# Kernel tuning notes

Hardware: AMD Instinct MI355X
Metric: run time of the kernel (lower is better)

The kernel has to match this reference:

```python
import jax, jax.numpy as jnp
import numpy as np

N = 50000
E = 800000
IN_DIM = 128
HID = 128
OUT = 40


def setup_inputs() -> dict:
    key = jax.random.key(0)
    k1, k2, k3, k4, k5 = jax.random.split(key, 5)
    x = jax.random.normal(k1, (N, IN_DIM), dtype=jnp.float32)
    edge_index = jax.random.randint(k2, (2, E), 0, N, dtype=jnp.int64)
    # Glorot-ish init for GCNConv weights, zero bias (PyG default bias=True)
    W1 = jax.random.normal(k3, (IN_DIM, HID), dtype=jnp.float32) / np.sqrt(IN_DIM)
    b1 = jnp.zeros((HID,), dtype=jnp.float32)
    W2 = jax.random.normal(k4, (HID, OUT), dtype=jnp.float32) / np.sqrt(HID)
    b2 = jnp.zeros((OUT,), dtype=jnp.float32)
    return {"x": x, "edge_index": edge_index, "W1": W1, "b1": b1, "W2": W2, "b2": b2}


def _gcn_norm(edge_index, n_nodes):
    """Add self-loops and compute symmetric GCN normalization per edge.
    Returns (src, dst, norm) with len E + n_nodes."""
    loops = jnp.arange(n_nodes, dtype=edge_index.dtype)
    src = jnp.concatenate([edge_index[0], loops])
    dst = jnpp_concat = jnp.concatenate([edge_index[1], loops])
    dst = jnp.concatenate([edge_index[1], loops])
    deg = jax.ops.segment_sum(jnp.ones_like(dst, dtype=jnp.float32), dst,
                              num_segments=n_nodes)
    dinv = jnp.where(deg > 0, jax.lax.rsqrt(deg), 0.0)
    norm = dinv[src] * dinv[dst]  # [E + N]
    return src, dst, norm


def _gcn_conv(x, src, dst, norm, W, b, n_nodes):
    xw = x @ W                                  # [N, F_out] transform first
    msg = xw[src] * norm[:, None]               # gather + scale, [E+N, F_out]
    out = jax.ops.segment_sum(msg, dst, num_segments=n_nodes)  # scatter-add
    return out + b


def reference(x, edge_index, W1, b1, W2, b2):
    n = x.shape[0]
    src, dst, norm = _gcn_norm(edge_index, n)
    h = _gcn_conv(x, src, dst, norm, W1, b1, n)
    h = jax.nn.relu(h)
    # dropout is identity in eval mode (training=False)
    h = _gcn_conv(h, src, dst, norm, W2, b2, n)
    return jax.nn.softmax(h, axis=1)
```

## Files before the change

kernel.cpp:

```cpp
#include <hip/hip_runtime.h>
#include <hip/hip_fp16.h>

#define IN_DIM 128
#define HID    128
#define OUTC   40
#define CAP    64
#define LSTR   136
#define CHUNK  4096
#define BINCAP 800

typedef _Float16 f16x8 __attribute__((ext_vector_type(8)));
typedef _Float16 f16x4 __attribute__((ext_vector_type(4)));
typedef float    f32x4 __attribute__((ext_vector_type(4)));

__device__ __forceinline__ int permi(int d, int NP8) { return (d & 7) * NP8 + (d >> 3); }

__global__ __launch_bounds__(256) void k_part(const int* __restrict__ edge, unsigned* __restrict__ staging,
                                              int* __restrict__ gcnt,
                                              const float* __restrict__ W1, const float* __restrict__ W2,
                                              _Float16* __restrict__ W1T, _Float16* __restrict__ W2T,
                                              int E, int n, int nbA, int ES8) {
  int b = blockIdx.x;
  if (b >= nbA) {
    int t = (b - nbA) * 256 + threadIdx.x;
    if (t < 128 * 128) {
      int nn = t >> 7, kk = t & 127;
      W1T[t] = (_Float16)W1[kk * 128 + nn];
    }
    if (t < 48 * 128) {
      int nn = t >> 7, kk = t & 127;
      W2T[t] = (nn < OUTC) ? (_Float16)W2[kk * OUTC + nn] : (_Float16)0.f;
    }
    return;
  }
  __shared__ unsigned lbin[8][BINCAP];
  __shared__ int lcnt[8];
  __shared__ int lbase[8];
  int tid = threadIdx.x;
  if (tid < 8) lcnt[tid] = 0;
  __syncthreads();
  int e0 = b * CHUNK;
#pragma unroll 4
  for (int i = 0; i < CHUNK / 256; ++i) {
    int e = e0 + i * 256 + tid;
    if (e < E) {
      int sv = edge[e];
      int d  = edge[E + e];
      if ((unsigned)d < (unsigned)n && (unsigned)sv < (unsigned)n) {
        int g = d & 7;
        unsigned pk = ((unsigned)(d >> 3) << 16) | (unsigned)sv;
        int p = atomicAdd(&lcnt[g], 1);
        if (p < BINCAP) lbin[g][p] = pk;
        else {
          int gp = atomicAdd(&gcnt[g], 1);
          staging[(size_t)g * ES8 + gp] = pk;
        }
      }
    }
  }
  __syncthreads();
  if (tid < 8) lbase[tid] = atomicAdd(&gcnt[tid], min(lcnt[tid], BINCAP));
  __syncthreads();
#pragma unroll
  for (int g = 0; g < 8; ++g) {
    int c = min(lcnt[g], BINCAP);
    int base = lbase[g];
    for (int idx = tid; idx < c; idx += 256)
      staging[(size_t)g * ES8 + base + idx] = lbin[g][idx];
  }
}

__global__ __launch_bounds__(256) void k_scat(const unsigned* __restrict__ staging, const int* __restrict__ gcnt,
                                              int* __restrict__ cnt, unsigned short* __restrict__ col,
                                              int NP8, int ES8) {
  int g = blockIdx.x & 7;
  int cE = gcnt[g];
  int t       = (blockIdx.x >> 3) * 256 + threadIdx.x;
  int gstride = (gridDim.x >> 3) * 256;
  const unsigned* sg = &staging[(size_t)g * ES8];
  for (int i = t; i < cE; i += gstride) {
    unsigned pk = sg[i];
    int p = g * NP8 + (int)(pk >> 16);
    int pos = atomicAdd(&cnt[p], 1);
    if (pos < CAP) col[(size_t)p * CAP + pos] = (unsigned short)(pk & 0xFFFFu);
  }
}


__global__ __launch_bounds__(256) void k_gemm1(const float* __restrict__ x, const _Float16* __restrict__ W1T,
                                               const int* __restrict__ cnt, __half* __restrict__ out,
                                               int n, int NP8) {
  __shared__ _Float16 sW[128 * LSTR];
  __shared__ _Float16 sX[64 * LSTR];
  int tid = threadIdx.x;
  int i0  = blockIdx.x * 64;

  {
    const uint4* src = (const uint4*)W1T;
    for (int idx = tid; idx < 2048; idx += 256) {
      int nn = idx >> 4, c = idx & 15;
      *(uint4*)&sW[nn * LSTR + c * 8] = src[nn * 16 + c];
    }
  }
  for (int idx = tid; idx < 2048; idx += 256) {
    int r = idx >> 5, c = idx & 31;
    int row = i0 + r;
    float4 v = (row < n) ? *(const float4*)&x[(size_t)row * IN_DIM + c * 4]
                         : make_float4(0.f, 0.f, 0.f, 0.f);
    f16x4 hv; hv[0] = (_Float16)v.x; hv[1] = (_Float16)v.y; hv[2] = (_Float16)v.z; hv[3] = (_Float16)v.w;
    *(f16x4*)&sX[r * LSTR + c * 4] = hv;
  }
  __syncthreads();

  int wv = tid >> 6, lane = tid & 63;
  int m = lane & 15, quad = lane >> 4;

  const _Float16* ax = &sX[(16 * wv + m) * LSTR + quad * 8];
  f16x8 a0 = *(const f16x8*)(ax);
  f16x8 a1 = *(const f16x8*)(ax + 32);
  f16x8 a2 = *(const f16x8*)(ax + 64);
  f16x8 a3 = *(const f16x8*)(ax + 96);

  int base_row = i0 + 16 * wv + quad * 4;
  float dvr[4];
#pragma unroll
  for (int r = 0; r < 4; ++r) {
    int row = base_row + r;
    dvr[r] = (row < n) ? rsqrtf((float)(cnt[permi(row, NP8)] + 1)) : 0.f;
  }

#pragma unroll
  for (int t = 0; t < 8; ++t) {
    const _Float16* bx = &sW[(t * 16 + m) * LSTR + quad * 8];
    f16x8 b0 = *(const f16x8*)(bx);
    f16x8 b1 = *(const f16x8*)(bx + 32);
    f16x8 b2 = *(const f16x8*)(bx + 64);
    f16x8 b3 = *(const f16x8*)(bx + 96);
    f32x4 c = {0.f, 0.f, 0.f, 0.f};
    c = __builtin_amdgcn_mfma_f32_16x16x32_f16(a0, b0, c, 0, 0, 0);
    c = __builtin_amdgcn_mfma_f32_16x16x32_f16(a1, b1, c, 0, 0, 0);
    c = __builtin_amdgcn_mfma_f32_16x16x32_f16(a2, b2, c, 0, 0, 0);
    c = __builtin_amdgcn_mfma_f32_16x16x32_f16(a3, b3, c, 0, 0, 0);
    int colb = t * 16 + m;
#pragma unroll
    for (int r = 0; r < 4; ++r) {
      int row = base_row + r;
      if (row < n) out[(size_t)row * HID + colb] = __float2half(c[r] * dvr[r]);
    }
  }
}


__global__ __launch_bounds__(256) void k_agg1(const __half2* __restrict__ xws, const int* __restrict__ cnt,
                                              const unsigned short* __restrict__ col, const float* __restrict__ b1,
                                              __half2* __restrict__ h, int n, int NP8) {
  int wid  = (blockIdx.x * 256 + threadIdx.x) >> 6;
  int lane = threadIdx.x & 63;
  if (wid >= n) return;
  float2 acc = __half22float2(xws[(size_t)wid * 64 + lane]);
  int p   = permi(wid, NP8);
  int deg = cnt[p];
  int end = min(deg, CAP);
  const unsigned short* cp = &col[(size_t)p * CAP];
  int e = 0;
  for (; e + 8 <= end; e += 8) {
    int s0 = cp[e], s1 = cp[e+1], s2 = cp[e+2], s3 = cp[e+3];
    int s4 = cp[e+4], s5 = cp[e+5], s6 = cp[e+6], s7 = cp[e+7];
    float2 v0 = __half22float2(xws[(size_t)s0 * 64 + lane]);
    float2 v1 = __half22float2(xws[(size_t)s1 * 64 + lane]);
    float2 v2 = __half22float2(xws[(size_t)s2 * 64 + lane]);
    float2 v3 = __half22float2(xws[(size_t)s3 * 64 + lane]);
    float2 v4 = __half22float2(xws[(size_t)s4 * 64 + lane]);
    float2 v5 = __half22float2(xws[(size_t)s5 * 64 + lane]);
    float2 v6 = __half22float2(xws[(size_t)s6 * 64 + lane]);
    float2 v7 = __half22float2(xws[(size_t)s7 * 64 + lane]);
    acc.x += (v0.x + v1.x) + (v2.x + v3.x) + ((v4.x + v5.x) + (v6.x + v7.x));
    acc.y += (v0.y + v1.y) + (v2.y + v3.y) + ((v4.y + v5.y) + (v6.y + v7.y));
  }
  for (; e < end; ++e) {
    float2 v = __half22float2(xws[(size_t)cp[e] * 64 + lane]);
    acc.x += v.x; acc.y += v.y;
  }
  float dv = rsqrtf((float)(deg + 1));
  float2 bb = ((const float2*)b1)[lane];
  h[(size_t)wid * 64 + lane] =
      __floats2half2_rn(fmaxf(acc.x * dv + bb.x, 0.f), fmaxf(acc.y * dv + bb.y, 0.f));
}


__global__ __launch_bounds__(256) void k_gemm2(const __half* __restrict__ h, const _Float16* __restrict__ W2T,
                                               const int* __restrict__ cnt, __half* __restrict__ out,
                                               int n, int NP8) {
  __shared__ _Float16 sW[48 * LSTR];
  __shared__ _Float16 sH[64 * LSTR];
  int tid = threadIdx.x;
  int i0  = blockIdx.x * 64;

  {
    const uint4* src = (const uint4*)W2T;
    for (int idx = tid; idx < 768; idx += 256) {
      int nn = idx >> 4, c = idx & 15;
      *(uint4*)&sW[nn * LSTR + c * 8] = src[nn * 16 + c];
    }
  }
  {
    const uint4* src = (const uint4*)h;
    for (int idx = tid; idx < 1024; idx += 256) {
      int r = idx >> 4, c = idx & 15;
      int row = i0 + r;
      uint4 v = (row < n) ? src[(size_t)row * 16 + c] : make_uint4(0u, 0u, 0u, 0u);
      *(uint4*)&sH[r * LSTR + c * 8] = v;
    }
  }
  __syncthreads();

  int wv = tid >> 6, lane = tid & 63;
  int m = lane & 15, quad = lane >> 4;

  const _Float16* ax = &sH[(16 * wv + m) * LSTR + quad * 8];
  f16x8 a0 = *(const f16x8*)(ax);
  f16x8 a1 = *(const f16x8*)(ax + 32);
  f16x8 a2 = *(const f16x8*)(ax + 64);
  f16x8 a3 = *(const f16x8*)(ax + 96);

  int base_row = i0 + 16 * wv + quad * 4;
  float dvr[4];
#pragma unroll
  for (int r = 0; r < 4; ++r) {
    int row = base_row + r;
    dvr[r] = (row < n) ? rsqrtf((float)(cnt[permi(row, NP8)] + 1)) : 0.f;
  }

#pragma unroll
  for (int t = 0; t < 3; ++t) {
    const _Float16* bx = &sW[(t * 16 + m) * LSTR + quad * 8];
    f16x8 b0 = *(const f16x8*)(bx);
    f16x8 b1 = *(const f16x8*)(bx + 32);
    f16x8 b2 = *(const f16x8*)(bx + 64);
    f16x8 b3 = *(const f16x8*)(bx + 96);
    f32x4 c = {0.f, 0.f, 0.f, 0.f};
    c = __builtin_amdgcn_mfma_f32_16x16x32_f16(a0, b0, c, 0, 0, 0);
    c = __builtin_amdgcn_mfma_f32_16x16x32_f16(a1, b1, c, 0, 0, 0);
    c = __builtin_amdgcn_mfma_f32_16x16x32_f16(a2, b2, c, 0, 0, 0);
    c = __builtin_amdgcn_mfma_f32_16x16x32_f16(a3, b3, c, 0, 0, 0);
    int colb = t * 16 + m;
    if (colb < OUTC) {
#pragma unroll
      for (int r = 0; r < 4; ++r) {
        int row = base_row + r;
        if (row < n) out[(size_t)row * OUTC + colb] = __float2half(c[r] * dvr[r]);
      }
    }
  }
}


__global__ __launch_bounds__(256) void k_agg2(const __half* __restrict__ hw, const int* __restrict__ cnt,
                                              const unsigned short* __restrict__ col, const float* __restrict__ b2,
                                              float* __restrict__ out, int n, int NP8) {
  int wid  = (blockIdx.x * 256 + threadIdx.x) >> 6;
  int lane = threadIdx.x & 63;
  if (wid >= n) return;
  bool act = lane < OUTC;
  int li = act ? lane : 0;
  float acc = act ? __half2float(hw[(size_t)wid * OUTC + li]) : 0.f;
  int p   = permi(wid, NP8);
  int deg = cnt[p];
  int end = min(deg, CAP);
  const unsigned short* cp = &col[(size_t)p * CAP];
  int e = 0;
  for (; e + 8 <= end; e += 8) {
    int s0 = cp[e], s1 = cp[e+1], s2 = cp[e+2], s3 = cp[e+3];
    int s4 = cp[e+4], s5 = cp[e+5], s6 = cp[e+6], s7 = cp[e+7];
    if (act) {
      float a0 = __half2float(hw[(size_t)s0 * OUTC + li]);
      float a1 = __half2float(hw[(size_t)s1 * OUTC + li]);
      float a2 = __half2float(hw[(size_t)s2 * OUTC + li]);
      float a3 = __half2float(hw[(size_t)s3 * OUTC + li]);
      float a4 = __half2float(hw[(size_t)s4 * OUTC + li]);
      float a5 = __half2float(hw[(size_t)s5 * OUTC + li]);
      float a6 = __half2float(hw[(size_t)s6 * OUTC + li]);
      float a7 = __half2float(hw[(size_t)s7 * OUTC + li]);
      acc += (a0 + a1) + (a2 + a3) + ((a4 + a5) + (a6 + a7));
    }
  }
  for (; e < end; ++e) {
    int s = cp[e];
    if (act) acc += __half2float(hw[(size_t)s * OUTC + li]);
  }
  float logit = acc * rsqrtf((float)(deg + 1)) + (act ? b2[lane] : 0.f);
  float m = act ? logit : -1e30f;
#pragma unroll
  for (int o = 32; o > 0; o >>= 1) m = fmaxf(m, __shfl_xor(m, o, 64));
  float ex = act ? __expf(logit - m) : 0.f;
  float sum = ex;
#pragma unroll
  for (int o = 32; o > 0; o >>= 1) sum += __shfl_xor(sum, o, 64);
  if (act) out[(size_t)wid * OUTC + lane] = ex / sum;
}


extern "C" void kernel_launch(void* const* d_in, const int* in_sizes, int n_in,
                              void* d_out, int out_size, void* d_ws, size_t ws_size,
                              hipStream_t stream) {
  const float* x    = (const float*)d_in[0];
  const int*   edge = (const int*)d_in[1];
  const float* W1   = (const float*)d_in[2];
  const float* b1   = (const float*)d_in[3];
  const float* W2   = (const float*)d_in[4];
  const float* b2   = (const float*)d_in[5];
  float* out = (float*)d_out;

  int N   = in_sizes[0] / IN_DIM;
  int E   = in_sizes[1] / 2;
  int NP8 = (N + 7) / 8;
  int NP  = NP8 * 8;
  int ES8 = E / 8 + 16384;

  char* ws = (char*)d_ws;
  size_t off = 0;
  auto carve = [&](size_t bytes) { char* p = ws + off; off = (off + bytes + 255) & ~(size_t)255; return p; };
  int*            gcnt    = (int*)carve(8 * 4);
  int*            cnt     = (int*)carve((size_t)NP * 4);
  unsigned*       staging = (unsigned*)carve((size_t)8 * ES8 * 4);
  unsigned short* col     = (unsigned short*)carve((size_t)NP * CAP * 2);
  _Float16*       W1T     = (_Float16*)carve((size_t)128 * 128 * 2);
  _Float16*       W2T     = (_Float16*)carve((size_t)48 * 128 * 2);
  __half*         xws     = (__half*)carve((size_t)N * HID * 2);
  __half*         h       = (__half*)carve((size_t)N * HID * 2);
  __half*         hw      = xws;

  hipMemsetAsync(gcnt, 0, (size_t)((char*)staging - (char*)gcnt), stream);

  int nbA = (E + CHUNK - 1) / CHUNK;
  k_part<<<nbA + 64, 256, 0, stream>>>(edge, staging, gcnt, W1, W2, W1T, W2T, E, N, nbA, ES8);
  k_scat<<<512, 256, 0, stream>>>(staging, gcnt, cnt, col, NP8, ES8);

  k_gemm1<<<(N + 63) / 64, 256, 0, stream>>>(x, W1T, cnt, xws, N, NP8);
  k_agg1<<<(N * 64 + 255) / 256, 256, 0, stream>>>((const __half2*)xws, cnt, col, b1, (__half2*)h, N, NP8);
  k_gemm2<<<(N + 63) / 64, 256, 0, stream>>>(h, W2T, cnt, hw, N, NP8);
  k_agg2<<<(N * 64 + 255) / 256, 256, 0, stream>>>(hw, cnt, col, b2, out, N, NP8);
}
```

Before: 222.5 us.

## Fuse edge partitioning with GEMM1 and aggregation1 with GEMM2

GEMM1 now runs in the same launch as edge partitioning, so it no longer scales by source degree. The missing scaling is applied per neighbor during aggregation by reading each source's degree. Layer-1 aggregation is fused with the layer-2 GEMM so the hidden activations stay in shared memory instead of round-tripping through global memory. A small init kernel replaces the memset, and the partition and GEMM1 work overlap in a single launch. In exchange, aggregation does an extra random cnt read and rsqrt per edge, and each block handles 64 rows with only 4 waves, which reduces parallelism for the gather.

```diff
diff --git a/kernel.cpp b/kernel.cpp
--- a/kernel.cpp
+++ b/kernel.cpp
@@ -15,58 +15,122 @@
 
 __device__ __forceinline__ int permi(int d, int NP8) { return (d & 7) * NP8 + (d >> 3); }
 
-__global__ __launch_bounds__(256) void k_part(const int* __restrict__ edge, unsigned* __restrict__ staging,
-                                              int* __restrict__ gcnt,
+__global__ __launch_bounds__(256) void k_init(int* __restrict__ cnt, int NP, int* __restrict__ gcnt,
                                               const float* __restrict__ W1, const float* __restrict__ W2,
-                                              _Float16* __restrict__ W1T, _Float16* __restrict__ W2T,
-                                              int E, int n, int nbA, int ES8) {
-  int b = blockIdx.x;
-  if (b >= nbA) {
-    int t = (b - nbA) * 256 + threadIdx.x;
-    if (t < 128 * 128) {
-      int nn = t >> 7, kk = t & 127;
-      W1T[t] = (_Float16)W1[kk * 128 + nn];
-    }
-    if (t < 48 * 128) {
-      int nn = t >> 7, kk = t & 127;
-      W2T[t] = (nn < OUTC) ? (_Float16)W2[kk * OUTC + nn] : (_Float16)0.f;
-    }
-    return;
-  }
-  __shared__ unsigned lbin[8][BINCAP];
-  __shared__ int lcnt[8];
-  __shared__ int lbase[8];
+                                              _Float16* __restrict__ W1T, _Float16* __restrict__ W2T) {
+  int t = blockIdx.x * 256 + threadIdx.x;
+  int stride = gridDim.x * 256;
+  for (int i = t; i < NP; i += stride) cnt[i] = 0;
+  if (t < 8) gcnt[t] = 0;
+  for (int i = t; i < 128 * 128; i += stride) {
+    int nn = i >> 7, kk = i & 127;
+    W1T[i] = (_Float16)W1[kk * 128 + nn];
+  }
+  for (int i = t; i < 48 * 128; i += stride) {
+    int nn = i >> 7, kk = i & 127;
+    W2T[i] = (nn < OUTC) ? (_Float16)W2[kk * OUTC + nn] : (_Float16)0.f;
+  }
+}
+
+#define SMEM_SZ 52224
+
+__global__ __launch_bounds__(256) void k_part_gemm1(const int* __restrict__ edge, unsigned* __restrict__ staging,
+                                                    int* __restrict__ gcnt,
+                                                    const float* __restrict__ x, const _Float16* __restrict__ W1T,
+                                                    __half* __restrict__ xws,
+                                                    int E, int n, int nbA, int ES8) {
+  __shared__ __align__(16) char smem[SMEM_SZ];
+  int b   = blockIdx.x;
   int tid = threadIdx.x;
-  if (tid < 8) lcnt[tid] = 0;
-  __syncthreads();
-  int e0 = b * CHUNK;
+
+  if (b < nbA) {
+    unsigned (*lbin)[BINCAP] = (unsigned (*)[BINCAP])smem;
+    int* lcnt  = (int*)(smem + 8 * BINCAP * 4);
+    int* lbase = lcnt + 8;
+    if (tid < 8) lcnt[tid] = 0;
+    __syncthreads();
+    int e0 = b * CHUNK;
 #pragma unroll 4
-  for (int i = 0; i < CHUNK / 256; ++i) {
-    int e = e0 + i * 256 + tid;
-    if (e < E) {
-      int sv = edge[e];
-      int d  = edge[E + e];
-      if ((unsigned)d < (unsigned)n && (unsigned)sv < (unsigned)n) {
-        int g = d & 7;
-        unsigned pk = ((unsigned)(d >> 3) << 16) | (unsigned)sv;
-        int p = atomicAdd(&lcnt[g], 1);
-        if (p < BINCAP) lbin[g][p] = pk;
-        else {
-          int gp = atomicAdd(&gcnt[g], 1);
-          staging[(size_t)g * ES8 + gp] = pk;
+    for (int i = 0; i < CHUNK / 256; ++i) {
+      int e = e0 + i * 256 + tid;
+      if (e < E) {
+        int sv = edge[e];
+        int d  = edge[E + e];
+        if ((unsigned)d < (unsigned)n && (unsigned)sv < (unsigned)n) {
+          int g = d & 7;
+          unsigned pk = ((unsigned)(d >> 3) << 16) | (unsigned)sv;
+          int p = atomicAdd(&lcnt[g], 1);
+          if (p < BINCAP) lbin[g][p] = pk;
+          else {
+            int gp = atomicAdd(&gcnt[g], 1);
+            staging[(size_t)g * ES8 + gp] = pk;
+          }
         }
       }
     }
+    __syncthreads();
+    if (tid < 8) lbase[tid] = atomicAdd(&gcnt[tid], min(lcnt[tid], BINCAP));
+    __syncthreads();
+#pragma unroll
+    for (int g = 0; g < 8; ++g) {
+      int c = min(lcnt[g], BINCAP);
+      int base = lbase[g];
+      for (int idx = tid; idx < c; idx += 256)
+        staging[(size_t)g * ES8 + base + idx] = lbin[g][idx];
+    }
+    return;
+  }
+
+  _Float16* sW = (_Float16*)smem;
+  _Float16* sX = (_Float16*)(smem + 128 * LSTR * 2);
+  int i0 = (b - nbA) * 64;
+
+  {
+    const uint4* src = (const uint4*)W1T;
+    for (int idx = tid; idx < 2048; idx += 256) {
+      int nn = idx >> 4, c = idx & 15;
+      *(uint4*)&sW[nn * LSTR + c * 8] = src[nn * 16 + c];
+    }
+  }
+  for (int idx = tid; idx < 2048; idx += 256) {
+    int r = idx >> 5, c = idx & 31;
+    int row = i0 + r;
+    float4 v = (row < n) ? *(const float4*)&x[(size_t)row * IN_DIM + c * 4]
+                         : make_float4(0.f, 0.f, 0.f, 0.f);
+    f16x4 hv; hv[0] = (_Float16)v.x; hv[1] = (_Float16)v.y; hv[2] = (_Float16)v.z; hv[3] = (_Float16)v.w;
+    *(f16x4*)&sX[r * LSTR + c * 4] = hv;
   }
   __syncthreads();
-  if (tid < 8) lbase[tid] = atomicAdd(&gcnt[tid], min(lcnt[tid], BINCAP));
-  __syncthreads();
-#pragma unroll
-  for (int g = 0; g < 8; ++g) {
-    int c = min(lcnt[g], BINCAP);
-    int base = lbase[g];
-    for (int idx = tid; idx < c; idx += 256)
-      staging[(size_t)g * ES8 + base + idx] = lbin[g][idx];
+
+  int wv = tid >> 6, lane = tid & 63;
+  int m = lane & 15, quad = lane >> 4;
+
+  const _Float16* ax = &sX[(16 * wv + m) * LSTR + quad * 8];
+  f16x8 a0 = *(const f16x8*)(ax);
+  f16x8 a1 = *(const f16x8*)(ax + 32);
+  f16x8 a2 = *(const f16x8*)(ax + 64);
+  f16x8 a3 = *(const f16x8*)(ax + 96);
+
+  int base_row = i0 + 16 * wv + quad * 4;
+
+#pragma unroll
+  for (int t = 0; t < 8; ++t) {
+    const _Float16* bx = &sW[(t * 16 + m) * LSTR + quad * 8];
+    f16x8 b0 = *(const f16x8*)(bx);
+    f16x8 b1 = *(const f16x8*)(bx + 32);
+    f16x8 b2 = *(const f16x8*)(bx + 64);
+    f16x8 b3 = *(const f16x8*)(bx + 96);
+    f32x4 c = {0.f, 0.f, 0.f, 0.f};
+    c = __builtin_amdgcn_mfma_f32_16x16x32_f16(a0, b0, c, 0, 0, 0);
+    c = __builtin_amdgcn_mfma_f32_16x16x32_f16(a1, b1, c, 0, 0, 0);
+    c = __builtin_amdgcn_mfma_f32_16x16x32_f16(a2, b2, c, 0, 0, 0);
+    c = __builtin_amdgcn_mfma_f32_16x16x32_f16(a3, b3, c, 0, 0, 0);
+    int colb = t * 16 + m;
+#pragma unroll
+    for (int r = 0; r < 4; ++r) {
+      int row = base_row + r;
+      if (row < n) xws[(size_t)row * HID + colb] = __float2half(c[r]);
+    }
   }
 }
 
@@ -87,112 +151,13 @@
 }
 
 
-__global__ __launch_bounds__(256) void k_gemm1(const float* __restrict__ x, const _Float16* __restrict__ W1T,
-                                               const int* __restrict__ cnt, __half* __restrict__ out,
-                                               int n, int NP8) {
-  __shared__ _Float16 sW[128 * LSTR];
-  __shared__ _Float16 sX[64 * LSTR];
-  int tid = threadIdx.x;
-  int i0  = blockIdx.x * 64;
-
-  {
-    const uint4* src = (const uint4*)W1T;
-    for (int idx = tid; idx < 2048; idx += 256) {
-      int nn = idx >> 4, c = idx & 15;
-      *(uint4*)&sW[nn * LSTR + c * 8] = src[nn * 16 + c];
-    }
-  }
-  for (int idx = tid; idx < 2048; idx += 256) {
-    int r = idx >> 5, c = idx & 31;
-    int row = i0 + r;
-    float4 v = (row < n) ? *(const float4*)&x[(size_t)row * IN_DIM + c * 4]
-                         : make_float4(0.f, 0.f, 0.f, 0.f);
-    f16x4 hv; hv[0] = (_Float16)v.x; hv[1] = (_Float16)v.y; hv[2] = (_Float16)v.z; hv[3] = (_Float16)v.w;
-    *(f16x4*)&sX[r * LSTR + c * 4] = hv;
-  }
-  __syncthreads();
-
-  int wv = tid >> 6, lane = tid & 63;
-  int m = lane & 15, quad = lane >> 4;
-
-  const _Float16* ax = &sX[(16 * wv + m) * LSTR + quad * 8];
-  f16x8 a0 = *(const f16x8*)(ax);
-  f16x8 a1 = *(const f16x8*)(ax + 32);
-  f16x8 a2 = *(const f16x8*)(ax + 64);
-  f16x8 a3 = *(const f16x8*)(ax + 96);
-
-  int base_row = i0 + 16 * wv + quad * 4;
-  float dvr[4];
-#pragma unroll
-  for (int r = 0; r < 4; ++r) {
-    int row = base_row + r;
-    dvr[r] = (row < n) ? rsqrtf((float)(cnt[permi(row, NP8)] + 1)) : 0.f;
-  }
-
-#pragma unroll
-  for (int t = 0; t < 8; ++t) {
-    const _Float16* bx = &sW[(t * 16 + m) * LSTR + quad * 8];
-    f16x8 b0 = *(const f16x8*)(bx);
-    f16x8 b1 = *(const f16x8*)(bx + 32);
-    f16x8 b2 = *(const f16x8*)(bx + 64);
-    f16x8 b3 = *(const f16x8*)(bx + 96);
-    f32x4 c = {0.f, 0.f, 0.f, 0.f};
-    c = __builtin_amdgcn_mfma_f32_16x16x32_f16(a0, b0, c, 0, 0, 0);
-    c = __builtin_amdgcn_mfma_f32_16x16x32_f16(a1, b1, c, 0, 0, 0);
-    c = __builtin_amdgcn_mfma_f32_16x16x32_f16(a2, b2, c, 0, 0, 0);
-    c = __builtin_amdgcn_mfma_f32_16x16x32_f16(a3, b3, c, 0, 0, 0);
-    int colb = t * 16 + m;
-#pragma unroll
-    for (int r = 0; r < 4; ++r) {
-      int row = base_row + r;
-      if (row < n) out[(size_t)row * HID + colb] = __float2half(c[r] * dvr[r]);
-    }
-  }
-}
-
-
-__global__ __launch_bounds__(256) void k_agg1(const __half2* __restrict__ xws, const int* __restrict__ cnt,
-                                              const unsigned short* __restrict__ col, const float* __restrict__ b1,
-                                              __half2* __restrict__ h, int n, int NP8) {
-  int wid  = (blockIdx.x * 256 + threadIdx.x) >> 6;
-  int lane = threadIdx.x & 63;
-  if (wid >= n) return;
-  float2 acc = __half22float2(xws[(size_t)wid * 64 + lane]);
-  int p   = permi(wid, NP8);
-  int deg = cnt[p];
-  int end = min(deg, CAP);
-  const unsigned short* cp = &col[(size_t)p * CAP];
-  int e = 0;
-  for (; e + 8 <= end; e += 8) {
-    int s0 = cp[e], s1 = cp[e+1], s2 = cp[e+2], s3 = cp[e+3];
-    int s4 = cp[e+4], s5 = cp[e+5], s6 = cp[e+6], s7 = cp[e+7];
-    float2 v0 = __half22float2(xws[(size_t)s0 * 64 + lane]);
-    float2 v1 = __half22float2(xws[(size_t)s1 * 64 + lane]);
-    float2 v2 = __half22float2(xws[(size_t)s2 * 64 + lane]);
-    float2 v3 = __half22float2(xws[(size_t)s3 * 64 + lane]);
-    float2 v4 = __half22float2(xws[(size_t)s4 * 64 + lane]);
-    float2 v5 = __half22float2(xws[(size_t)s5 * 64 + lane]);
-    float2 v6 = __half22float2(xws[(size_t)s6 * 64 + lane]);
-    float2 v7 = __half22float2(xws[(size_t)s7 * 64 + lane]);
-    acc.x += (v0.x + v1.x) + (v2.x + v3.x) + ((v4.x + v5.x) + (v6.x + v7.x));
-    acc.y += (v0.y + v1.y) + (v2.y + v3.y) + ((v4.y + v5.y) + (v6.y + v7.y));
-  }
-  for (; e < end; ++e) {
-    float2 v = __half22float2(xws[(size_t)cp[e] * 64 + lane]);
-    acc.x += v.x; acc.y += v.y;
-  }
-  float dv = rsqrtf((float)(deg + 1));
-  float2 bb = ((const float2*)b1)[lane];
-  h[(size_t)wid * 64 + lane] =
-      __floats2half2_rn(fmaxf(acc.x * dv + bb.x, 0.f), fmaxf(acc.y * dv + bb.y, 0.f));
-}
-
-
-__global__ __launch_bounds__(256) void k_gemm2(const __half* __restrict__ h, const _Float16* __restrict__ W2T,
-                                               const int* __restrict__ cnt, __half* __restrict__ out,
-                                               int n, int NP8) {
+__global__ __launch_bounds__(256) void k_agg1_gemm2(const __half2* __restrict__ xws, const int* __restrict__ cnt,
+                                                    const unsigned short* __restrict__ col,
+                                                    const float* __restrict__ b1, const _Float16* __restrict__ W2T,
+                                                    __half* __restrict__ hw, int n, int NP8) {
   __shared__ _Float16 sW[48 * LSTR];
   __shared__ _Float16 sH[64 * LSTR];
+  __shared__ float sDV[64];
   int tid = threadIdx.x;
   int i0  = blockIdx.x * 64;
 
@@ -203,20 +168,49 @@
       *(uint4*)&sW[nn * LSTR + c * 8] = src[nn * 16 + c];
     }
   }
-  {
-    const uint4* src = (const uint4*)h;
-    for (int idx = tid; idx < 1024; idx += 256) {
-      int r = idx >> 4, c = idx & 15;
-      int row = i0 + r;
-      uint4 v = (row < n) ? src[(size_t)row * 16 + c] : make_uint4(0u, 0u, 0u, 0u);
-      *(uint4*)&sH[r * LSTR + c * 8] = v;
-    }
-  }
   __syncthreads();
 
   int wv = tid >> 6, lane = tid & 63;
+  float2 bb = ((const float2*)b1)[lane];
+
+  for (int j = 0; j < 16; ++j) {
+    int rloc = 16 * wv + j;
+    int wid  = i0 + rloc;
+    if (wid >= n) continue;
+    int p   = permi(wid, NP8);
+    int deg = cnt[p];
+    float dvd = rsqrtf((float)(deg + 1));
+    if (lane == 0) sDV[rloc] = dvd;
+    float2 sv = __half22float2(xws[(size_t)wid * 64 + lane]);
+    float2 acc; acc.x = sv.x * dvd; acc.y = sv.y * dvd;
+    int end = min(deg, CAP);
+    const unsigned short* cp = &col[(size_t)p * CAP];
+    int e = 0;
+    for (; e + 4 <= end; e += 4) {
+      int s0 = cp[e], s1 = cp[e+1], s2 = cp[e+2], s3 = cp[e+3];
+      float d0 = rsqrtf((float)(cnt[permi(s0, NP8)] + 1));
+      float d1 = rsqrtf((float)(cnt[permi(s1, NP8)] + 1));
+      float d2 = rsqrtf((float)(cnt[permi(s2, NP8)] + 1));
+      float d3 = rsqrtf((float)(cnt[permi(s3, NP8)] + 1));
+      float2 v0 = __half22float2(xws[(size_t)s0 * 64 + lane]);
+      float2 v1 = __half22float2(xws[(size_t)s1 * 64 + lane]);
+      float2 v2 = __half22float2(xws[(size_t)s2 * 64 + lane]);
+      float2 v3 = __half22float2(xws[(size_t)s3 * 64 + lane]);
+      acc.x += v0.x * d0 + v1.x * d1 + v2.x * d2 + v3.x * d3;
+      acc.y += v0.y * d0 + v1.y * d1 + v2.y * d2 + v3.y * d3;
+    }
+    for (; e < end; ++e) {
+      int s = cp[e];
+      float ds = rsqrtf((float)(cnt[permi(s, NP8)] + 1));
+      float2 v = __half22float2(xws[(size_t)s * 64 + lane]);
+      acc.x += v.x * ds; acc.y += v.y * ds;
+    }
+    float hx = fmaxf(acc.x * dvd + bb.x, 0.f);
+    float hy = fmaxf(acc.y * dvd + bb.y, 0.f);
+    *(__half2*)&sH[rloc * LSTR + 2 * lane] = __floats2half2_rn(hx, hy);
+  }
+
   int m = lane & 15, quad = lane >> 4;
-
   const _Float16* ax = &sH[(16 * wv + m) * LSTR + quad * 8];
   f16x8 a0 = *(const f16x8*)(ax);
   f16x8 a1 = *(const f16x8*)(ax + 32);
@@ -224,12 +218,6 @@
   f16x8 a3 = *(const f16x8*)(ax + 96);
 
   int base_row = i0 + 16 * wv + quad * 4;
-  float dvr[4];
-#pragma unroll
-  for (int r = 0; r < 4; ++r) {
-    int row = base_row + r;
-    dvr[r] = (row < n) ? rsqrtf((float)(cnt[permi(row, NP8)] + 1)) : 0.f;
-  }
 
 #pragma unroll
   for (int t = 0; t < 3; ++t) {
@@ -248,7 +236,7 @@
 #pragma unroll
       for (int r = 0; r < 4; ++r) {
         int row = base_row + r;
-        if (row < n) out[(size_t)row * OUTC + colb] = __float2half(c[r] * dvr[r]);
+        if (row < n) hw[(size_t)row * OUTC + colb] = __float2half(c[r] * sDV[16 * wv + quad * 4 + r]);
       }
     }
   }
@@ -327,17 +315,14 @@
   _Float16*       W1T     = (_Float16*)carve((size_t)128 * 128 * 2);
   _Float16*       W2T     = (_Float16*)carve((size_t)48 * 128 * 2);
   __half*         xws     = (__half*)carve((size_t)N * HID * 2);
-  __half*         h       = (__half*)carve((size_t)N * HID * 2);
-  __half*         hw      = xws;
-
-  hipMemsetAsync(gcnt, 0, (size_t)((char*)staging - (char*)gcnt), stream);
+  __half*         hw      = (__half*)carve((size_t)N * OUTC * 2);
 
   int nbA = (E + CHUNK - 1) / CHUNK;
-  k_part<<<nbA + 64, 256, 0, stream>>>(edge, staging, gcnt, W1, W2, W1T, W2T, E, N, nbA, ES8);
+  int nbG = (N + 63) / 64;
+
+  k_init<<<64, 256, 0, stream>>>(cnt, NP, gcnt, W1, W2, W1T, W2T);
+  k_part_gemm1<<<nbA + nbG, 256, 0, stream>>>(edge, staging, gcnt, x, W1T, xws, E, N, nbA, ES8);
   k_scat<<<512, 256, 0, stream>>>(staging, gcnt, cnt, col, NP8, ES8);
-
-  k_gemm1<<<(N + 63) / 64, 256, 0, stream>>>(x, W1T, cnt, xws, N, NP8);
-  k_agg1<<<(N * 64 + 255) / 256, 256, 0, stream>>>((const __half2*)xws, cnt, col, b1, (__half2*)h, N, NP8);
-  k_gemm2<<<(N + 63) / 64, 256, 0, stream>>>(h, W2T, cnt, hw, N, NP8);
+  k_agg1_gemm2<<<nbG, 256, 0, stream>>>((const __half2*)xws, cnt, col, b1, W2T, hw, N, NP8);
   k_agg2<<<(N * 64 + 255) / 256, 256, 0, stream>>>(hw, cnt, col, b2, out, N, NP8);
 }
```

Measured after the change: 248.9 us. 1.12x slower.
